# Optimization experiments

Measured on AMD Instinct MI355X. Metric: run time of the kernel, lower is better.

The kernel has to match this reference:

```python
import jax, jax.numpy as jnp
import numpy as np


def conv1d(x, w, b, pad):
    # x: (B, Cin, T), w: (Cout, Cin, K), b: (Cout,)
    y = jax.lax.conv_general_dilated(x, w, window_strides=(1,), padding=[(pad, pad)],
                                     dimension_numbers=('NCH', 'OIH', 'NCH'))
    return y + b[None, :, None]


def setup_inputs() -> dict:
    key = jax.random.key(0)
    ks = jax.random.split(key, 12)
    B, Cm, T1, Ct, T2, Ca = 8, 80, 800, 512, 200, 80
    queries = jax.random.normal(ks[0], (B, Cm, T1), dtype=jnp.float32)
    keys = jax.random.normal(ks[1], (B, Ct, T2), dtype=jnp.float32)
    query_lens = jnp.full((B,), T1, dtype=jnp.int32)
    key_lens = jax.random.randint(ks[2], (B,), T2 // 2, T2 + 1)
    # mask True where key position is padding (>= key_len): (B, T2, 1)
    mask = (jnp.arange(T2)[None, :] >= key_lens[:, None])[:, :, None]
    attn_prior = jax.random.uniform(ks[3], (B, T1, T2), dtype=jnp.float32) + 0.1
    # key_proj: Conv1d(512->1024, k=3, pad=1) + ReLU + Conv1d(1024->80, k=1)
    kp_w1 = jax.random.normal(ks[4], (2 * Ct, Ct, 3), jnp.float32) * 0.02
    kp_b1 = jnp.zeros((2 * Ct,), jnp.float32)
    kp_w2 = jax.random.normal(ks[5], (Ca, 2 * Ct, 1), jnp.float32) * 0.02
    kp_b2 = jnp.zeros((Ca,), jnp.float32)
    # query_proj (3xconv): Conv1d(80->160,k3)+ReLU+Conv1d(160->80,k1)+ReLU+Conv1d(80->80,k1)
    qp_w1 = jax.random.normal(ks[6], (2 * Cm, Cm, 3), jnp.float32) * 0.05
    qp_b1 = jnp.zeros((2 * Cm,), jnp.float32)
    qp_w2 = jax.random.normal(ks[7], (Cm, 2 * Cm, 1), jnp.float32) * 0.05
    qp_b2 = jnp.zeros((Cm,), jnp.float32)
    qp_w3 = jax.random.normal(ks[8], (Ca, Cm, 1), jnp.float32) * 0.05
    qp_b3 = jnp.zeros((Ca,), jnp.float32)
    return {"queries": queries, "keys": keys, "query_lens": query_lens, "mask": mask,
            "attn_prior": attn_prior, "kp_w1": kp_w1, "kp_b1": kp_b1, "kp_w2": kp_w2,
            "kp_b2": kp_b2, "qp_w1": qp_w1, "qp_b1": qp_b1, "qp_w2": qp_w2,
            "qp_b2": qp_b2, "qp_w3": qp_w3, "qp_b3": qp_b3}


def reference(queries, keys, query_lens, mask, attn_prior,
              kp_w1, kp_b1, kp_w2, kp_b2,
              qp_w1, qp_b1, qp_w2, qp_b2, qp_w3, qp_b3):
    # key projection: (B, Ct, T2) -> (B, Ca, T2)
    ke = conv1d(keys, kp_w1, kp_b1, pad=1)
    ke = jax.nn.relu(ke)
    ke = conv1d(ke, kp_w2, kp_b2, pad=0)
    # query projection ('3xconv'): (B, Cm, T1) -> (B, Ca, T1)
    qe = conv1d(queries, qp_w1, qp_b1, pad=1)
    qe = jax.nn.relu(qe)
    qe = conv1d(qe, qp_w2, qp_b2, pad=0)
    qe = jax.nn.relu(qe)
    qe = conv1d(qe, qp_w3, qp_b3, pad=0)
    # broadcasted squared L2 distance: (B, Ca, T1, T2) -> reduce C -> (B, 1, T1, T2)
    diff2 = (qe[:, :, :, None] - ke[:, :, None, :]) ** 2
    attn = -0.0005 * jnp.sum(diff2, axis=1, keepdims=True)
    # prior in log domain
    attn = jax.nn.log_softmax(attn, axis=3) + jnp.log(attn_prior[:, None] + 1e-8)
    attn_logprob = attn
    # mask (B, T2, 1) -> (B, 1, 1, T2)
    m = jnp.transpose(mask, (0, 2, 1))[:, :, None, :]
    attn = jnp.where(m, -jnp.inf, attn)
    attn = jax.nn.softmax(attn, axis=3)
    return (attn, attn_logprob)
```

## Files before the change

### kernel.cpp

```cpp
#include <hip/hip_runtime.h>
#include <hip/hip_bf16.h>
#include <math.h>

#define B_  8
#define CM  80
#define T1_ 800
#define CT  512
#define T2_ 200
#define CA  80

using bf16 = __hip_bfloat16;
typedef __attribute__((ext_vector_type(8))) short bf16x8;
typedef __attribute__((ext_vector_type(4))) float f32x4;

#define LDSW 56
#define LDSW2 72
#define LDSW3 168
#define LDSW4 104

__device__ __forceinline__ float load_sel(const void* p, long idx, int isf32) {
  if (isf32) return ((const float*)p)[idx];
  return __bfloat162float(((const bf16*)p)[idx]);
}

__device__ __forceinline__ unsigned short f2bf(float x) {
  bf16 h = __float2bfloat16(x);
  return *reinterpret_cast<unsigned short*>(&h);
}

__device__ __forceinline__ int detect_f32(const unsigned short* q) {
  __shared__ int s_f;
  const int tid = threadIdx.x;
  if (tid < 64) {
    unsigned short u = q[2 * tid];
    int e = (u >> 7) & 0xFF;
    unsigned long long bal = __ballot(e < 100 || e > 154);
    if (tid == 0) s_f = (__popcll(bal) >= 16) ? 1 : 0;
  }
  __syncthreads();
  return s_f;
}

__device__ void task_cvt_t(const void* X, bf16* XT, int f, int C, int T,
                           int id2, int tilesT, float* smem, int tid) {
  const int per_b = tilesT * ((C + 31) >> 5);
  const int b = id2 / per_b;
  const int r = id2 - b * per_b;
  const int ct = r / tilesT, tt = r - ct * tilesT;
  const int c0 = ct * 32, t0 = tt * 32;
  const int tx = tid & 31, trow = tid >> 5;
#pragma unroll
  for (int p = 0; p < 4; ++p) {
    const int cr = trow + 8 * p;
    if (c0 + cr < C && t0 + tx < T)
      smem[cr * 33 + tx] = load_sel(X, ((long)b * C + c0 + cr) * T + t0 + tx, f);
  }
  __syncthreads();
#pragma unroll
  for (int p = 0; p < 4; ++p) {
    const int tr = trow + 8 * p;
    if (t0 + tr < T && c0 + tx < C)
      XT[((long)b * T + t0 + tr) * C + c0 + tx] =
          __float2bfloat16(smem[tx * 33 + tr]);
  }
}

__device__ void task_wfrag(const void* W, bf16* WF, int f, int id2, int tid) {
  const int id = id2 * 256 + tid;
  const int l  = id & 63;
  int rest = id >> 6;
  const int h  = rest & 1; rest >>= 1;
  const int mi = rest & 3; rest >>= 2;
  const int w2 = rest & 1; rest >>= 1;
  const int ks = rest % 24;
  const int p  = rest / 24;
  const int co = p * 128 + w2 * 64 + mi * 16 + (l & 15);
  const int k0 = ks * 64 + h * 32 + (l >> 4) * 8;
  const int dk = k0 >> 9;
  const int ci = k0 & 511;
  const long sbase = ((long)co * 512 + ci) * 3 + dk;
  ushort4 u0, u1;
  u0.x = f2bf(load_sel(W, sbase + 0 * 3, f));
  u0.y = f2bf(load_sel(W, sbase + 1 * 3, f));
  u0.z = f2bf(load_sel(W, sbase + 2 * 3, f));
  u0.w = f2bf(load_sel(W, sbase + 3 * 3, f));
  u1.x = f2bf(load_sel(W, sbase + 4 * 3, f));
  u1.y = f2bf(load_sel(W, sbase + 5 * 3, f));
  u1.z = f2bf(load_sel(W, sbase + 6 * 3, f));
  u1.w = f2bf(load_sel(W, sbase + 7 * 3, f));
  *(ushort4*)(WF + (long)id * 8) = u0;
  *(ushort4*)(WF + (long)id * 8 + 4) = u1;
}

__device__ void task_wt3v(const void* W, bf16* WT, int f, int Co, int Ci,
                          int id2, int tid) {
  const int i = id2 * 256 + tid;
  const int g4 = Ci >> 2;
  if (i >= Co * g4) return;
  const int co = i / g4, ci = (i - co * g4) * 4;
  const long sbase = ((long)co * Ci + ci) * 3;
  float w[12];
  if (f) {
    const float4* s = (const float4*)((const float*)W + sbase);
    float4 f0 = s[0], f1 = s[1], f2 = s[2];
    w[0]=f0.x; w[1]=f0.y; w[2]=f0.z; w[3]=f0.w; w[4]=f1.x; w[5]=f1.y;
    w[6]=f1.z; w[7]=f1.w; w[8]=f2.x; w[9]=f2.y; w[10]=f2.z; w[11]=f2.w;
  } else {
#pragma unroll
    for (int j = 0; j < 12; ++j) w[j] = load_sel(W, sbase + j, 0);
  }
#pragma unroll
  for (int dk = 0; dk < 3; ++dk) {
    ushort4 u;
    u.x = f2bf(w[0 * 3 + dk]); u.y = f2bf(w[1 * 3 + dk]);
    u.z = f2bf(w[2 * 3 + dk]); u.w = f2bf(w[3 * 3 + dk]);
    *(ushort4*)(WT + ((long)dk * Co + co) * Ci + ci) = u;
  }
}

__device__ void task_cvtv(const void* W, bf16* O, int f, int n, int id2, int tid) {
  const int i = (id2 * 256 + tid) * 4;
  if (i >= n) return;
  ushort4 u;
  if (f) {
    float4 v = *(const float4*)((const float*)W + i);
    u.x = f2bf(v.x); u.y = f2bf(v.y); u.z = f2bf(v.z); u.w = f2bf(v.w);
  } else {
    u.x = f2bf(load_sel(W, i, 0));     u.y = f2bf(load_sel(W, i + 1, 0));
    u.z = f2bf(load_sel(W, i + 2, 0)); u.w = f2bf(load_sel(W, i + 3, 0));
  }
  *(ushort4*)(O + i) = u;
}

__global__ __launch_bounds__(256) void k_prep(
    const void* __restrict__ queries, const void* __restrict__ keys,
    const void* __restrict__ mask,
    const void* __restrict__ kp_w1, const void* __restrict__ kp_b1,
    const void* __restrict__ kp_w2, const void* __restrict__ kp_b2,
    const void* __restrict__ qp_w1, const void* __restrict__ qp_b1,
    const void* __restrict__ qp_w2, const void* __restrict__ qp_b2,
    const void* __restrict__ qp_w3, const void* __restrict__ qp_b3,
    bf16* __restrict__ keysT, bf16* __restrict__ queriesT,
    bf16* __restrict__ w1F, bf16* __restrict__ qw1T,
    bf16* __restrict__ kw2c, bf16* __restrict__ qw2c, bf16* __restrict__ qw3c,
    float* __restrict__ biasf, float* __restrict__ mf, float* __restrict__ kn) {
  __shared__ float smem[32 * 33];
  const int tid = threadIdx.x;
  const int f = detect_f32((const unsigned short*)queries);
  int id = blockIdx.x;

  if (id < 896) { task_cvt_t(keys, keysT, f, CT, T2_, id, 7, smem, tid); return; }
  id -= 896;
  if (id < 600) { task_cvt_t(queries, queriesT, f, CM, T1_, id, 25, smem, tid); return; }
  id -= 600;
  if (id < 768) { task_wfrag(kp_w1, w1F, f, id, tid); return; }
  id -= 768;
  if (id < 13) { task_wt3v(qp_w1, qw1T, f, 160, CM, id, tid); return; }
  id -= 13;
  if (id < 80) { task_cvtv(kp_w2, kw2c, f, 80 * 1024, id, tid); return; }
  id -= 80;
  if (id < 13) { task_cvtv(qp_w2, qw2c, f, 80 * 160, id, tid); return; }
  id -= 13;
  if (id < 7) { task_cvtv(qp_w3, qw3c, f, 80 * 80, id, tid); return; }
  id -= 7;

  if (id == 0) {
    for (int i = tid; i < 1424; i += 256) {
      float v;
      if (i < 1024)      v = load_sel(kp_b1, i, f);
      else if (i < 1104) v = load_sel(kp_b2, i - 1024, f);
      else if (i < 1264) v = load_sel(qp_b1, i - 1104, f);
      else if (i < 1344) v = load_sel(qp_b2, i - 1264, f);
      else               v = load_sel(qp_b3, i - 1344, f);
      biasf[i] = v;
    }
    for (int i = tid; i < B_ * T2_; i += 256) kn[i] = 0.f;
    return;
  }

  {
    int* s_fmt = (int*)smem;
    const int nmask = B_ * T2_;
    if (tid == 0) s_fmt[0] = 1;
    __syncthreads();
    const unsigned int* wi = (const unsigned int*)mask;
    const int nw = nmask / 4;
    int pri = 0;
    for (int i = tid; i < nw; i += 256) {
      unsigned int w = wi[i];
      if (w == 0u || w == 1u) continue;
      if (w == 0x3F803F80u || w == 0x00003F80u) { pri = max(pri, 2); continue; }
      if (w == 0x3F800000u) continue;
      unsigned int b0 = w & 0xFFu, b1 = (w >> 8) & 0xFFu,
                   b2 = (w >> 16) & 0xFFu, b3 = (w >> 24) & 0xFFu;
      if (b0 <= 1u && b1 <= 1u && b2 <= 1u && b3 <= 1u) pri = max(pri, 3);
      else pri = max(pri, 2);
    }
    if (pri) atomicMax(&s_fmt[0], pri);
    __syncthreads();
    const int fmt = s_fmt[0];
    for (int i = tid; i < nmask; i += 256) {
      int m;
      if (fmt == 3)      m = ((const unsigned char*)mask)[i] != 0;
      else if (fmt == 2) m = ((const unsigned short*)mask)[i] != 0;
      else               m = (wi[i] != 0u);
      mf[i] = (float)m;
    }
  }
}

__device__ void conv_tile(
    const bf16* __restrict__ XT, const bf16* __restrict__ WT,
    const float* __restrict__ bias, void* __restrict__ Y,
    int Cin, int Cout, int T, int KW, int pad, int relu, int outmode,
    int m0, int n0, short* As, short* Bs, float* Y2 = nullptr) {
  const int K = Cin * KW;
  const int tid = threadIdx.x;
  const int wave = tid >> 6;
  const int lane = tid & 63;

  const int row = tid >> 2;
  const int koff = (tid & 3) * 8;
  const int n = n0 + row;
  const int bb = n / T;
  const int t = n - bb * T;

  const int wm = (wave >> 1) * 32;
  const int wn = (wave & 1) * 32;
  const int fm = lane & 15;
  const int quad = lane >> 4;

  f32x4 acc[2][2] = {};

  const short* ap0 = As + (wm + fm) * LDSW + quad * 8;
  const short* bp0 = Bs + (wn + fm) * LDSW + quad * 8;

  auto loadA = [&](int k0) -> uint4 {
    const int k = k0 + koff;
    const int m = m0 + row;
    uint4 v = {0u, 0u, 0u, 0u};
    if (m < Cout && k < K) {
      const int dk = k / Cin;
      const int ci = k - dk * Cin;
      v = *(const uint4*)(WT + ((long)dk * Cout + m) * Cin + ci);
    }
    return v;
  };
  auto loadB = [&](int k0) -> uint4 {
    const int k = k0 + koff;
    uint4 v = {0u, 0u, 0u, 0u};
    if (k < K) {
      const int dk = k / Cin;
      const int ci = k - dk * Cin;
      const int tt = t + dk - pad;
      if (tt >= 0 && tt < T)
        v = *(const uint4*)(XT + ((long)bb * T + tt) * Cin + ci);
    }
    return v;
  };

  uint4 va = loadA(0);
  uint4 vb = loadB(0);

  for (int k0 = 0; k0 < K; k0 += 32) {
    *(uint4*)(As + row * LDSW + koff) = va;
    *(uint4*)(Bs + row * LDSW + koff) = vb;
    if (k0 + 32 < K) {
      va = loadA(k0 + 32);
      vb = loadB(k0 + 32);
    }
    __syncthreads();
    {
      bf16x8 a0 = *(const bf16x8*)(ap0);
      bf16x8 a1 = *(const bf16x8*)(ap0 + 16 * LDSW);
      bf16x8 b0 = *(const bf16x8*)(bp0);
      bf16x8 b1 = *(const bf16x8*)(bp0 + 16 * LDSW);
      acc[0][0] = __builtin_amdgcn_mfma_f32_16x16x32_bf16(a0, b0, acc[0][0], 0, 0, 0);
      acc[0][1] = __builtin_amdgcn_mfma_f32_16x16x32_bf16(a0, b1, acc[0][1], 0, 0, 0);
      acc[1][0] = __builtin_amdgcn_mfma_f32_16x16x32_bf16(a1, b0, acc[1][0], 0, 0, 0);
      acc[1][1] = __builtin_amdgcn_mfma_f32_16x16x32_bf16(a1, b1, acc[1][1], 0, 0, 0);
    }
    __syncthreads();
  }

#pragma unroll
  for (int mi = 0; mi < 2; ++mi) {
    const int mrow = m0 + wm + mi * 16 + quad * 4;
    if (mrow >= Cout) continue;
    float bi[4];
#pragma unroll
    for (int r = 0; r < 4; ++r) bi[r] = bias[mrow + r];
#pragma unroll
    for (int ni = 0; ni < 2; ++ni) {
      const int ncol = n0 + wn + ni * 16 + fm;
      float o[4];
#pragma unroll
      for (int r = 0; r < 4; ++r) {
        float v = acc[mi][ni][r] + bi[r];
        if (relu) v = fmaxf(v, 0.f);
        o[r] = v;
      }
      if (outmode == 0) {
        ushort4 u;
        u.x = f2bf(o[0]); u.y = f2bf(o[1]); u.z = f2bf(o[2]); u.w = f2bf(o[3]);
        *(ushort4*)((bf16*)Y + (long)ncol * Cout + mrow) = u;
      } else if (outmode == 1) {
        *(float4*)((float*)Y + (long)ncol * Cout + mrow) =
            make_float4(o[0], o[1], o[2], o[3]);
      } else {
        const int bb2 = ncol / T;
        const int tloc = ncol - bb2 * T;
        float s4 = 0.f;
#pragma unroll
        for (int r = 0; r < 4; ++r) {
          ((float*)Y)[((long)bb2 * Cout + mrow + r) * T + tloc] = -2.f * o[r];
          s4 = fmaf(o[r], o[r], s4);
        }
        atomicAdd(&Y2[ncol], s4);
      }
    }
  }
}

__device__ void conv_key128(
    const bf16* __restrict__ XT, const bf16* __restrict__ WF,
    const float* __restrict__ bias, bf16* __restrict__ Y,
    int panel, int n0, short* Bs) {
  const int Cin = CT, Cout = 1024, T = T2_;
  const int tid = threadIdx.x;
  const int wave = tid >> 6;
  const int lane = tid & 63;
  const int m0 = panel * 128;

  const int rowb = tid >> 2;
  const int nb = n0 + rowb;
  const int bbb = nb / T;
  const int tb = nb - bbb * T;
  const int kcb = (tid & 3) * 16;

  const int w2 = wave >> 1;
  const int wn = (wave & 1) * 32;
  const int fm = lane & 15;
  const int quad = lane >> 4;

  f32x4 acc[4][2] = {};
  const short* bp0 = Bs + (wn + fm) * LDSW2 + quad * 8;

  uint4 vb0, vb1;
  auto loadB = [&](int k0) {
    const int dk = k0 >> 9;
    const int ci0 = k0 & 511;
    const int tt = tb + dk - 1;
    if (tt >= 0 && tt < T) {
      const bf16* src = XT + ((long)bbb * T + tt) * Cin + ci0 + kcb;
      vb0 = *(const uint4*)(src);
      vb1 = *(const uint4*)(src + 8);
    } else {
      uint4 z = {0u, 0u, 0u, 0u};
      vb0 = z; vb1 = z;
    }
  };

  bf16x8 a0c[4], a1c[4], a0n[4], a1n[4];
  auto loadA = [&](int ks, bf16x8 d0[4], bf16x8 d1[4]) {
    const long abase = ((((long)panel * 24 + ks) * 2 + w2) * 4096) + lane * 8;
#pragma unroll
    for (int mi = 0; mi < 4; ++mi) {
      d0[mi] = *(const bf16x8*)(WF + abase + (mi * 2 + 0) * 512);
      d1[mi] = *(const bf16x8*)(WF + abase + (mi * 2 + 1) * 512);
    }
  };

  loadB(0);
  loadA(0, a0c, a1c);

  for (int k0 = 0; k0 < 1536; k0 += 64) {
    {
      short* dstb = Bs + rowb * LDSW2 + kcb;
      *(uint4*)(dstb) = vb0;
      *(uint4*)(dstb + 8) = vb1;
    }
    const bool more = (k0 + 64 < 1536);
    if (more) {
      loadB(k0 + 64);
      loadA((k0 >> 6) + 1, a0n, a1n);
    }
    __syncthreads();
    {
      bf16x8 b00 = *(const bf16x8*)(bp0);
      bf16x8 b01 = *(const bf16x8*)(bp0 + 16 * LDSW2);
#pragma unroll
      for (int mi = 0; mi < 4; ++mi) {
        acc[mi][0] = __builtin_amdgcn_mfma_f32_16x16x32_bf16(a0c[mi], b00, acc[mi][0], 0, 0, 0);
        acc[mi][1] = __builtin_amdgcn_mfma_f32_16x16x32_bf16(a0c[mi], b01, acc[mi][1], 0, 0, 0);
      }
      bf16x8 b10 = *(const bf16x8*)(bp0 + 32);
      bf16x8 b11 = *(const bf16x8*)(bp0 + 16 * LDSW2 + 32);
#pragma unroll
      for (int mi = 0; mi < 4; ++mi) {
        acc[mi][0] = __builtin_amdgcn_mfma_f32_16x16x32_bf16(a1c[mi], b10, acc[mi][0], 0, 0, 0);
        acc[mi][1] = __builtin_amdgcn_mfma_f32_16x16x32_bf16(a1c[mi], b11, acc[mi][1], 0, 0, 0);
      }
    }
    __syncthreads();
    if (more) {
#pragma unroll
      for (int mi = 0; mi < 4; ++mi) { a0c[mi] = a0n[mi]; a1c[mi] = a1n[mi]; }
    }
  }

#pragma unroll
  for (int mi = 0; mi < 4; ++mi) {
    const int mrow = m0 + w2 * 64 + mi * 16 + quad * 4;
    float bi[4];
#pragma unroll
    for (int r = 0; r < 4; ++r) bi[r] = bias[mrow + r];
#pragma unroll
    for (int ni = 0; ni < 2; ++ni) {
      const int ncol = n0 + wn + ni * 16 + fm;
      const long base = (long)ncol * Cout + mrow;
      ushort4 u;
      u.x = f2bf(fmaxf(acc[mi][ni][0] + bi[0], 0.f));
      u.y = f2bf(fmaxf(acc[mi][ni][1] + bi[1], 0.f));
      u.z = f2bf(fmaxf(acc[mi][ni][2] + bi[2], 0.f));
      u.w = f2bf(fmaxf(acc[mi][ni][3] + bi[3], 0.f));
      *(ushort4*)(Y + base) = u;
    }
  }
}

__global__ __launch_bounds__(256) void k_conv1(
    const bf16* __restrict__ keysT, const bf16* __restrict__ w1F,
    const float* __restrict__ b_k1, bf16* __restrict__ ke1T,
    const bf16* __restrict__ queriesT, const bf16* __restrict__ qw1T,
    const float* __restrict__ b_q1, bf16* __restrict__ qe1T) {
  __shared__ __align__(16) short smem[2 * 64 * LDSW];
  int j = blockIdx.x;
  if (j < 200) {
    conv_key128(keysT, w1F, b_k1, ke1T, j & 7, (j >> 3) * 64, smem);
  } else {
    j -= 200;
    conv_tile(queriesT, qw1T, b_q1, qe1T, CM, 160, T1_, 3, 1, 1, 0,
              (j / 100) * 64, (j % 100) * 64, smem, smem + 64 * LDSW);
  }
}

__device__ void conv23_tile(
    const bf16* __restrict__ qe1T, const bf16* __restrict__ qw2c,
    const float* __restrict__ b_q2, const bf16* __restrict__ qw3c,
    const float* __restrict__ b_q3, float* __restrict__ qeT,
    float* __restrict__ qn, int n0, short* smem) {
  short* sIn = smem;
  short* sW2 = smem + 64 * LDSW3;
  short* sC  = smem;
  short* sW3 = smem + 64 * LDSW3;
  const int tid = threadIdx.x;
  const int wave = tid >> 6;
  const int lane = tid & 63;
  const int fm = lane & 15;
  const int quad = lane >> 4;

#pragma unroll
  for (int c = tid; c < 1280; c += 256) {
    const int row = c / 20, kc = (c - row * 20) * 8;
    uint4 v = *(const uint4*)(qe1T + (long)(n0 + row) * 160 + kc);
    *(uint4*)(sIn + row * LDSW3 + kc) = v;
  }
  for (int c = tid; c < 1600; c += 256) {
    const int row = c / 20, kc = (c - row * 20) * 8;
    uint4 v = *(const uint4*)(qw2c + (long)row * 160 + kc);
    *(uint4*)(sW2 + row * LDSW3 + kc) = v;
  }
  __syncthreads();

  f32x4 acc1[5] = {};
#pragma unroll
  for (int ks = 0; ks < 5; ++ks) {
    bf16x8 b = *(const bf16x8*)(sIn + (16 * wave + fm) * LDSW3 + ks * 32 + quad * 8);
#pragma unroll
    for (int mt = 0; mt < 5; ++mt) {
      bf16x8 a = *(const bf16x8*)(sW2 + (16 * mt + fm) * LDSW3 + ks * 32 + quad * 8);
      acc1[mt] = __builtin_amdgcn_mfma_f32_16x16x32_bf16(a, b, acc1[mt], 0, 0, 0);
    }
  }
  __syncthreads();

#pragma unroll
  for (int mt = 0; mt < 5; ++mt) {
    const int ch = 16 * mt + quad * 4;
    const float4 b2 = *(const float4*)(b_q2 + ch);
    ushort4 u;
    u.x = f2bf(fmaxf(acc1[mt][0] + b2.x, 0.f));
    u.y = f2bf(fmaxf(acc1[mt][1] + b2.y, 0.f));
    u.z = f2bf(fmaxf(acc1[mt][2] + b2.z, 0.f));
    u.w = f2bf(fmaxf(acc1[mt][3] + b2.w, 0.f));
    *(ushort4*)(sC + (16 * wave + fm) * LDSW4 + ch) = u;
  }
  if (tid < 128) {
    const int row = tid >> 1, off = 80 + (tid & 1) * 8;
    uint4 z = {0u, 0u, 0u, 0u};
    *(uint4*)(sC + row * LDSW4 + off) = z;
  }
  for (int c = tid; c < 800; c += 256) {
    const int row = c / 10, kc = (c - row * 10) * 8;
    uint4 v = *(const uint4*)(qw3c + (long)row * 80 + kc);
    *(uint4*)(sW3 + row * LDSW4 + kc) = v;
  }
  if (tid < 160) {
    const int row = tid >> 1, off = 80 + (tid & 1) * 8;
    uint4 z = {0u, 0u, 0u, 0u};
    *(uint4*)(sW3 + row * LDSW4 + off) = z;
  }
  __syncthreads();

  f32x4 acc2[5] = {};
#pragma unroll
  for (int ks = 0; ks < 3; ++ks) {
    bf16x8 b = *(const bf16x8*)(sC + (16 * wave + fm) * LDSW4 + ks * 32 + quad * 8);
#pragma unroll
    for (int mt = 0; mt < 5; ++mt) {
      bf16x8 a = *(const bf16x8*)(sW3 + (16 * mt + fm) * LDSW4 + ks * 32 + quad * 8);
      acc2[mt] = __builtin_amdgcn_mfma_f32_16x16x32_bf16(a, b, acc2[mt], 0, 0, 0);
    }
  }

  const int pos = n0 + 16 * wave + fm;
  float p = 0.f;
#pragma unroll
  for (int mt = 0; mt < 5; ++mt) {
    const int ch = 16 * mt + quad * 4;
    const float4 b3 = *(const float4*)(b_q3 + ch);
    float4 o = make_float4(acc2[mt][0] + b3.x, acc2[mt][1] + b3.y,
                           acc2[mt][2] + b3.z, acc2[mt][3] + b3.w);
    p = fmaf(o.x, o.x, p); p = fmaf(o.y, o.y, p);
    p = fmaf(o.z, o.z, p); p = fmaf(o.w, o.w, p);
    *(float4*)(qeT + (long)pos * CA + ch) = o;
  }
  p += __shfl_xor(p, 16, 64);
  p += __shfl_xor(p, 32, 64);
  if (quad == 0) qn[pos] = p;
}

__global__ __launch_bounds__(256) void k_conv2f(
    const bf16* __restrict__ ke1T, const bf16* __restrict__ kw2c,
    const float* __restrict__ b_k2, float* __restrict__ keT,
    float* __restrict__ kn,
    const bf16* __restrict__ qe1T, const bf16* __restrict__ qw2c,
    const float* __restrict__ b_q2, const bf16* __restrict__ qw3c,
    const float* __restrict__ b_q3, float* __restrict__ qeT,
    float* __restrict__ qn) {
  __shared__ __align__(16) short smem[64 * LDSW3 + 80 * LDSW3];
  int j = blockIdx.x;
  if (j < 50) {
    conv_tile(ke1T, kw2c, b_k2, keT, 1024, CA, T2_, 1, 0, 0, 2,
              (j / 25) * 64, (j % 25) * 64, smem, smem + 64 * LDSW, kn);
  } else {
    conv23_tile(qe1T, qw2c, b_q2, qw3c, b_q3, qeT, qn, (j - 50) * 64, smem);
  }
}

__global__ __launch_bounds__(256) void k_dist(
    const float* __restrict__ qeT, const float* __restrict__ keT2,
    const float* __restrict__ kn, const float* __restrict__ qn,
    const void* __restrict__ prior, const float* __restrict__ mf,
    void* __restrict__ out, const unsigned short* __restrict__ qprobe) {
  __shared__ float sq[4 * CA];
  __shared__ float sqn[4];
  __shared__ float redA[16], redB[16], redC[16], redD[16];
  const int f = detect_f32(qprobe);
  const int b = blockIdx.y;
  const int t1base = blockIdx.x * 4;
  const int tid = threadIdx.x;
  const int wid = tid >> 6;

  const int t2 = tid;
  const bool valid = (t2 < T2_);
  const long N = (long)B_ * T1_ * T2_;

  float pr[4] = {0.f, 0.f, 0.f, 0.f};
  float mval = 1.f;
  if (valid) {
#pragma unroll
    for (int u = 0; u < 4; ++u)
      pr[u] = load_sel(prior, ((long)b * T1_ + t1base + u) * T2_ + t2, f);
    mval = mf[b * T2_ + t2];
  }

  for (int i = tid; i < 4 * CA; i += 256) {
    int u = i / CA, c = i - u * CA;
    sq[i] = qeT[((long)b * T1_ + t1base + u) * CA + c];
  }
  if (tid < 4) sqn[tid] = qn[b * T1_ + t1base + tid];
  __syncthreads();

  float x[4] = {-INFINITY, -INFINITY, -INFINITY, -INFINITY};
  if (valid) {
    const float* kp = keT2 + (long)b * CA * T2_ + t2;
    const float knv = kn[b * T2_ + t2];
    float a0 = 0.f, a1 = 0.f, a2 = 0.f, a3 = 0.f;
#pragma unroll 2
    for (int j = 0; j < CA; j += 4) {
      const float4 q0 = *(const float4*)(sq + 0 * CA + j);
      const float4 q1 = *(const float4*)(sq + 1 * CA + j);
      const float4 q2 = *(const float4*)(sq + 2 * CA + j);
      const float4 q3 = *(const float4*)(sq + 3 * CA + j);
      const float k0v = kp[(j + 0) * T2_];
      const float k1v = kp[(j + 1) * T2_];
      const float k2v = kp[(j + 2) * T2_];
      const float k3v = kp[(j + 3) * T2_];
      a0 = fmaf(k0v, q0.x, a0); a0 = fmaf(k1v, q0.y, a0);
      a0 = fmaf(k2v, q0.z, a0); a0 = fmaf(k3v, q0.w, a0);
      a1 = fmaf(k0v, q1.x, a1); a1 = fmaf(k1v, q1.y, a1);
      a1 = fmaf(k2v, q1.z, a1); a1 = fmaf(k3v, q1.w, a1);
      a2 = fmaf(k0v, q2.x, a2); a2 = fmaf(k1v, q2.y, a2);
      a2 = fmaf(k2v, q2.z, a2); a2 = fmaf(k3v, q2.w, a2);
      a3 = fmaf(k0v, q3.x, a3); a3 = fmaf(k1v, q3.y, a3);
      a3 = fmaf(k2v, q3.z, a3); a3 = fmaf(k3v, q3.w, a3);
    }
    x[0] = -0.0005f * (a0 + sqn[0] + knv);
    x[1] = -0.0005f * (a1 + sqn[1] + knv);
    x[2] = -0.0005f * (a2 + sqn[2] + knv);
    x[3] = -0.0005f * (a3 + sqn[3] + knv);
  }

  float y[4], ym[4];
#pragma unroll
  for (int u = 0; u < 4; ++u) {
    if (valid) {
      const float lpr = __logf(fmaxf(pr[u], 0.f) + 1e-8f);
      y[u] = x[u] + lpr;
    } else {
      y[u] = -INFINITY;
    }
    ym[u] = (valid && mval == 0.f) ? y[u] : -INFINITY;
  }

  float m1[4], m2[4];
#pragma unroll
  for (int u = 0; u < 4; ++u) { m1[u] = x[u]; m2[u] = ym[u]; }
#pragma unroll
  for (int o = 32; o > 0; o >>= 1)
#pragma unroll
    for (int u = 0; u < 4; ++u) {
      m1[u] = fmaxf(m1[u], __shfl_down(m1[u], o, 64));
      m2[u] = fmaxf(m2[u], __shfl_down(m2[u], o, 64));
    }
  if ((tid & 63) == 0)
#pragma unroll
    for (int u = 0; u < 4; ++u) {
      redA[wid * 4 + u] = m1[u];
      redB[wid * 4 + u] = m2[u];
    }
  __syncthreads();
  float M1[4], M2[4];
#pragma unroll
  for (int u = 0; u < 4; ++u) {
    M1[u] = fmaxf(fmaxf(redA[u], redA[4 + u]), fmaxf(redA[8 + u], redA[12 + u]));
    M2[u] = fmaxf(fmaxf(redB[u], redB[4 + u]), fmaxf(redB[8 + u], redB[12 + u]));
  }

  float e2[4], s1[4], s2[4];
#pragma unroll
  for (int u = 0; u < 4; ++u) {
    s1[u] = (x[u] == -INFINITY) ? 0.f : __expf(x[u] - M1[u]);
    e2[u] = (ym[u] == -INFINITY) ? 0.f : __expf(ym[u] - M2[u]);
    s2[u] = e2[u];
  }
#pragma unroll
  for (int o = 32; o > 0; o >>= 1)
#pragma unroll
    for (int u = 0; u < 4; ++u) {
      s1[u] += __shfl_down(s1[u], o, 64);
      s2[u] += __shfl_down(s2[u], o, 64);
    }
  if ((tid & 63) == 0)
#pragma unroll
    for (int u = 0; u < 4; ++u) {
      redC[wid * 4 + u] = s1[u];
      redD[wid * 4 + u] = s2[u];
    }
  __syncthreads();

#pragma unroll
  for (int u = 0; u < 4; ++u) {
    const float S1 = redC[u] + redC[4 + u] + redC[8 + u] + redC[12 + u];
    const float S2 = redD[u] + redD[4 + u] + redD[8 + u] + redD[12 + u];
    if (valid) {
      const float logZ = __logf(S1);
      const float lp = y[u] - M1[u] - logZ;
      const float a = (S2 > 0.f) ? (e2[u] / S2) : 0.f;
      const long oidx = ((long)b * T1_ + t1base + u) * T2_ + t2;
      if (f) {
        ((float*)out)[N + oidx] = lp;
        ((float*)out)[oidx] = a;
      } else {
        ((bf16*)out)[N + oidx] = __float2bfloat16(lp);
        ((bf16*)out)[oidx] = __float2bfloat16(a);
      }
    }
  }
}

extern "C" void kernel_launch(void* const* d_in, const int* in_sizes, int n_in,
                              void* d_out, int out_size, void* d_ws, size_t ws_size,
                              hipStream_t stream) {
  const void* queries = d_in[0];
  const void* keys    = d_in[1];
  const void* mask    = d_in[3];
  const void* prior   = d_in[4];
  const void* kp_w1 = d_in[5];
  const void* kp_b1 = d_in[6];
  const void* kp_w2 = d_in[7];
  const void* kp_b2 = d_in[8];
  const void* qp_w1 = d_in[9];
  const void* qp_b1 = d_in[10];
  const void* qp_w2 = d_in[11];
  const void* qp_b2 = d_in[12];
  const void* qp_w3 = d_in[13];
  const void* qp_b3 = d_in[14];

  float* keT   = (float*)d_ws;
  float* qeT   = keT + 128000;
  float* mf    = qeT + 512000;
  float* biasf = mf + 1600;
  float* kn    = biasf + 1440;
  float* qn    = kn + 1600;
  bf16* keysT    = (bf16*)(qn + 6400);
  bf16* queriesT = keysT + 819200;
  bf16* w1F      = queriesT + 512000;
  bf16* qw1T     = w1F + 1572864;
  bf16* kw2c     = qw1T + 38400;
  bf16* qw2c     = kw2c + 81920;
  bf16* qw3c     = qw2c + 12800;
  bf16* ke1T     = qw3c + 6400;
  bf16* qe1T     = ke1T + 1638400;

  float* b_k1 = biasf;
  float* b_k2 = biasf + 1024;
  float* b_q1 = biasf + 1104;
  float* b_q2 = biasf + 1264;
  float* b_q3 = biasf + 1344;

  k_prep<<<2379, 256, 0, stream>>>(
      queries, keys, mask,
      kp_w1, kp_b1, kp_w2, kp_b2,
      qp_w1, qp_b1, qp_w2, qp_b2, qp_w3, qp_b3,
      keysT, queriesT, w1F, qw1T, kw2c, qw2c, qw3c, biasf, mf, kn);

  k_conv1<<<500, 256, 0, stream>>>(keysT, w1F, b_k1, ke1T,
                                   queriesT, qw1T, b_q1, qe1T);

  k_conv2f<<<150, 256, 0, stream>>>(ke1T, kw2c, b_k2, keT, kn,
                                    qe1T, qw2c, b_q2, qw3c, b_q3, qeT, qn);

  k_dist<<<dim3(200, B_), 256, 0, stream>>>(
      qeT, keT, kn, qn, prior, mf, d_out, (const unsigned short*)queries);
}
```

Before: 148.1 us.

## Fuse conv1 and conv2/3 kernels into one persistent kernel with grid barrier

Merges the two convolution-stage launches into a single 512-block kernel separated by a software grid barrier built on an atomic counter that is zeroed with a memset before launch. The goal is to remove one kernel launch and the inter-kernel gap. In exchange it adds a memset, an atomic spin barrier, and the requirement that all 512 blocks are resident at the same time or the kernel deadlocks. The shared-memory array is also enlarged to cover both phases, which may lower occupancy.

```diff
diff --git a/kernel.cpp b/kernel.cpp
--- a/kernel.cpp
+++ b/kernel.cpp
@@ -17,6 +17,8 @@
 #define LDSW2 72
 #define LDSW3 168
 #define LDSW4 104
+
+#define NBLK 512
 
 __device__ __forceinline__ float load_sel(const void* p, long idx, int isf32) {
   if (isf32) return ((const float*)p)[idx];
@@ -39,6 +41,19 @@
   }
   __syncthreads();
   return s_f;
+}
+
+__device__ __forceinline__ void grid_bar(int* cnt) {
+  __syncthreads();
+  if (threadIdx.x == 0) {
+    __threadfence();
+    int arrived = atomicAdd(cnt, 1) + 1;
+    if (arrived < NBLK) {
+      while (atomicAdd(cnt, 0) < NBLK) __builtin_amdgcn_s_sleep(4);
+    }
+    __threadfence();
+  }
+  __syncthreads();
 }
 
 __device__ void task_cvt_t(const void* X, bf16* XT, int f, int C, int T,
@@ -429,22 +444,6 @@
   }
 }
 
-__global__ __launch_bounds__(256) void k_conv1(
-    const bf16* __restrict__ keysT, const bf16* __restrict__ w1F,
-    const float* __restrict__ b_k1, bf16* __restrict__ ke1T,
-    const bf16* __restrict__ queriesT, const bf16* __restrict__ qw1T,
-    const float* __restrict__ b_q1, bf16* __restrict__ qe1T) {
-  __shared__ __align__(16) short smem[2 * 64 * LDSW];
-  int j = blockIdx.x;
-  if (j < 200) {
-    conv_key128(keysT, w1F, b_k1, ke1T, j & 7, (j >> 3) * 64, smem);
-  } else {
-    j -= 200;
-    conv_tile(queriesT, qw1T, b_q1, qe1T, CM, 160, T1_, 3, 1, 1, 0,
-              (j / 100) * 64, (j % 100) * 64, smem, smem + 64 * LDSW);
-  }
-}
-
 __device__ void conv23_tile(
     const bf16* __restrict__ qe1T, const bf16* __restrict__ qw2c,
     const float* __restrict__ b_q2, const bf16* __restrict__ qw3c,
@@ -541,20 +540,34 @@
   if (quad == 0) qn[pos] = p;
 }
 
-__global__ __launch_bounds__(256) void k_conv2f(
-    const bf16* __restrict__ ke1T, const bf16* __restrict__ kw2c,
-    const float* __restrict__ b_k2, float* __restrict__ keT,
-    float* __restrict__ kn,
-    const bf16* __restrict__ qe1T, const bf16* __restrict__ qw2c,
-    const float* __restrict__ b_q2, const bf16* __restrict__ qw3c,
-    const float* __restrict__ b_q3, float* __restrict__ qeT,
-    float* __restrict__ qn) {
-  __shared__ __align__(16) short smem[64 * LDSW3 + 80 * LDSW3];
-  int j = blockIdx.x;
+__global__ __launch_bounds__(256, 2) void k_convs(
+    const bf16* __restrict__ keysT, const bf16* __restrict__ w1F,
+    const float* __restrict__ b_k1, bf16* __restrict__ ke1T,
+    const bf16* __restrict__ queriesT, const bf16* __restrict__ qw1T,
+    const float* __restrict__ b_q1, bf16* __restrict__ qe1T,
+    const bf16* __restrict__ kw2c, const float* __restrict__ b_k2,
+    float* __restrict__ keT, float* __restrict__ kn,
+    const bf16* __restrict__ qw2c, const float* __restrict__ b_q2,
+    const bf16* __restrict__ qw3c, const float* __restrict__ b_q3,
+    float* __restrict__ qeT, float* __restrict__ qn,
+    int* __restrict__ bars) {
+  __shared__ __align__(16) short smem[144 * LDSW3];
+  const int j = blockIdx.x;
+
+  if (j < 200) {
+    conv_key128(keysT, w1F, b_k1, ke1T, j & 7, (j >> 3) * 64, smem);
+  } else if (j < 500) {
+    const int q = j - 200;
+    conv_tile(queriesT, qw1T, b_q1, qe1T, CM, 160, T1_, 3, 1, 1, 0,
+              (q / 100) * 64, (q % 100) * 64, smem, smem + 64 * LDSW);
+  }
+
+  grid_bar(&bars[0]);
+
   if (j < 50) {
     conv_tile(ke1T, kw2c, b_k2, keT, 1024, CA, T2_, 1, 0, 0, 2,
               (j / 25) * 64, (j % 25) * 64, smem, smem + 64 * LDSW, kn);
-  } else {
+  } else if (j < 150) {
     conv23_tile(qe1T, qw2c, b_q2, qw3c, b_q3, qeT, qn, (j - 50) * 64, smem);
   }
 }
@@ -741,17 +754,18 @@
   float* b_q2 = biasf + 1264;
   float* b_q3 = biasf + 1344;
 
+  int* bars = (int*)((char*)d_ws + (200u << 20));
+  hipMemsetAsync(bars, 0, 64, stream);
+
   k_prep<<<2379, 256, 0, stream>>>(
       queries, keys, mask,
       kp_w1, kp_b1, kp_w2, kp_b2,
       qp_w1, qp_b1, qp_w2, qp_b2, qp_w3, qp_b3,
       keysT, queriesT, w1F, qw1T, kw2c, qw2c, qw3c, biasf, mf, kn);
 
-  k_conv1<<<500, 256, 0, stream>>>(keysT, w1F, b_k1, ke1T,
-                                   queriesT, qw1T, b_q1, qe1T);
-
-  k_conv2f<<<150, 256, 0, stream>>>(ke1T, kw2c, b_k2, keT, kn,
-                                    qe1T, qw2c, b_q2, qw3c, b_q3, qeT, qn);
+  k_convs<<<NBLK, 256, 0, stream>>>(
+      keysT, w1F, b_k1, ke1T, queriesT, qw1T, b_q1, qe1T,
+      kw2c, b_k2, keT, kn, qw2c, b_q2, qw3c, b_q3, qeT, qn, bars);
 
   k_dist<<<dim3(200, B_), 256, 0, stream>>>(
       qeT, keT, kn, qn, prior, mf, d_out, (const unsigned short*)queries);
```

New measurement: 207.6 us. +40.2%, slower.

## Double key-conv K-step to 128 per barrier pair with ping-pong A registers

Applied to the files above, without the earlier changes.

The key projection conv GEMM now stages 128 K elements of B per LDS round instead of 64, which halves the number of __syncthreads pairs. A fragments alternate between two register sets, so the copy between them at the end of each step is gone, and the next A load is issued midway through the MFMA work. In exchange the kernel uses more LDS (a wider padded row) and more registers for staging B.

```diff
diff --git a/kernel.cpp b/kernel.cpp
--- a/kernel.cpp
+++ b/kernel.cpp
@@ -14,7 +14,7 @@
 typedef __attribute__((ext_vector_type(4))) float f32x4;
 
 #define LDSW 56
-#define LDSW2 72
+#define LDSW2B 136
 #define LDSW3 168
 #define LDSW4 104
 
@@ -336,7 +336,7 @@
   const int nb = n0 + rowb;
   const int bbb = nb / T;
   const int tb = nb - bbb * T;
-  const int kcb = (tid & 3) * 16;
+  const int kcb = (tid & 3) * 32;
 
   const int w2 = wave >> 1;
   const int wn = (wave & 1) * 32;
@@ -344,20 +344,21 @@
   const int quad = lane >> 4;
 
   f32x4 acc[4][2] = {};
-  const short* bp0 = Bs + (wn + fm) * LDSW2 + quad * 8;
-
-  uint4 vb0, vb1;
+  const short* bp0 = Bs + (wn + fm) * LDSW2B + quad * 8;
+
+  uint4 vb[4];
   auto loadB = [&](int k0) {
     const int dk = k0 >> 9;
     const int ci0 = k0 & 511;
     const int tt = tb + dk - 1;
     if (tt >= 0 && tt < T) {
       const bf16* src = XT + ((long)bbb * T + tt) * Cin + ci0 + kcb;
-      vb0 = *(const uint4*)(src);
-      vb1 = *(const uint4*)(src + 8);
+#pragma unroll
+      for (int r = 0; r < 4; ++r) vb[r] = *(const uint4*)(src + r * 8);
     } else {
       uint4 z = {0u, 0u, 0u, 0u};
-      vb0 = z; vb1 = z;
+#pragma unroll
+      for (int r = 0; r < 4; ++r) vb[r] = z;
     }
   };
 
@@ -374,39 +375,51 @@
   loadB(0);
   loadA(0, a0c, a1c);
 
-  for (int k0 = 0; k0 < 1536; k0 += 64) {
+  for (int K0 = 0; K0 < 1536; K0 += 128) {
+    const int ks0 = K0 >> 6;
     {
-      short* dstb = Bs + rowb * LDSW2 + kcb;
-      *(uint4*)(dstb) = vb0;
-      *(uint4*)(dstb + 8) = vb1;
-    }
-    const bool more = (k0 + 64 < 1536);
-    if (more) {
-      loadB(k0 + 64);
-      loadA((k0 >> 6) + 1, a0n, a1n);
-    }
+      short* dstb = Bs + rowb * LDSW2B + kcb;
+#pragma unroll
+      for (int r = 0; r < 4; ++r) *(uint4*)(dstb + r * 8) = vb[r];
+    }
+    const bool more = (K0 + 128 < 1536);
+    if (more) loadB(K0 + 128);
+    loadA(ks0 + 1, a0n, a1n);
     __syncthreads();
     {
       bf16x8 b00 = *(const bf16x8*)(bp0);
-      bf16x8 b01 = *(const bf16x8*)(bp0 + 16 * LDSW2);
+      bf16x8 b01 = *(const bf16x8*)(bp0 + 16 * LDSW2B);
 #pragma unroll
       for (int mi = 0; mi < 4; ++mi) {
         acc[mi][0] = __builtin_amdgcn_mfma_f32_16x16x32_bf16(a0c[mi], b00, acc[mi][0], 0, 0, 0);
         acc[mi][1] = __builtin_amdgcn_mfma_f32_16x16x32_bf16(a0c[mi], b01, acc[mi][1], 0, 0, 0);
       }
       bf16x8 b10 = *(const bf16x8*)(bp0 + 32);
-      bf16x8 b11 = *(const bf16x8*)(bp0 + 16 * LDSW2 + 32);
+      bf16x8 b11 = *(const bf16x8*)(bp0 + 16 * LDSW2B + 32);
 #pragma unroll
       for (int mi = 0; mi < 4; ++mi) {
         acc[mi][0] = __builtin_amdgcn_mfma_f32_16x16x32_bf16(a1c[mi], b10, acc[mi][0], 0, 0, 0);
         acc[mi][1] = __builtin_amdgcn_mfma_f32_16x16x32_bf16(a1c[mi], b11, acc[mi][1], 0, 0, 0);
       }
     }
+    if (more) loadA(ks0 + 2, a0c, a1c);
+    {
+      bf16x8 b20 = *(const bf16x8*)(bp0 + 64);
+      bf16x8 b21 = *(const bf16x8*)(bp0 + 16 * LDSW2B + 64);
+#pragma unroll
+      for (int mi = 0; mi < 4; ++mi) {
+        acc[mi][0] = __builtin_amdgcn_mfma_f32_16x16x32_bf16(a0n[mi], b20, acc[mi][0], 0, 0, 0);
+        acc[mi][1] = __builtin_amdgcn_mfma_f32_16x16x32_bf16(a0n[mi], b21, acc[mi][1], 0, 0, 0);
+      }
+      bf16x8 b30 = *(const bf16x8*)(bp0 + 96);
+      bf16x8 b31 = *(const bf16x8*)(bp0 + 16 * LDSW2B + 96);
+#pragma unroll
+      for (int mi = 0; mi < 4; ++mi) {
+        acc[mi][0] = __builtin_amdgcn_mfma_f32_16x16x32_bf16(a1n[mi], b30, acc[mi][0], 0, 0, 0);
+        acc[mi][1] = __builtin_amdgcn_mfma_f32_16x16x32_bf16(a1n[mi], b31, acc[mi][1], 0, 0, 0);
+      }
+    }
     __syncthreads();
-    if (more) {
-#pragma unroll
-      for (int mi = 0; mi < 4; ++mi) { a0c[mi] = a0n[mi]; a1c[mi] = a1n[mi]; }
-    }
   }
 
 #pragma unroll
@@ -434,7 +447,7 @@
     const float* __restrict__ b_k1, bf16* __restrict__ ke1T,
     const bf16* __restrict__ queriesT, const bf16* __restrict__ qw1T,
     const float* __restrict__ b_q1, bf16* __restrict__ qe1T) {
-  __shared__ __align__(16) short smem[2 * 64 * LDSW];
+  __shared__ __align__(16) short smem[64 * LDSW2B];
   int j = blockIdx.x;
   if (j < 200) {
     conv_key128(keysT, w1F, b_k1, ke1T, j & 7, (j >> 3) * 64, smem);
```

Result: no change. 147.1 us (-0.6%).
